# Kernel optimization log

Measured on AMD Instinct MI355X. Metric: run time of the kernel, lower is better.

The kernel has to match this reference:

```python
import jax, jax.numpy as jnp
from jax import lax
import numpy as np

D_MODEL = 128
N_HEADS = 8
N_POINTS = 8
MAX_MAG = 10.0
NEG_SLOPE = 0.1


def conv2d(x, w, b, pad):
    # x: (N, Cin, H, W), w: (Cout, Cin, kh, kw)
    y = lax.conv_general_dilated(x, w, (1, 1), [(pad, pad), (pad, pad)],
                                 dimension_numbers=('NCHW', 'OIHW', 'NCHW'))
    return y + b[None, :, None, None]


def leaky(x):
    return jnp.where(x >= 0, x, NEG_SLOPE * x)


def bilinear_sample(img, grid):
    # img: (B, C, H, W); grid: (B, P, H, W, 2) in [-1, 1] (x, y)
    # Matches torch F.grid_sample(mode='bilinear', padding_mode='zeros', align_corners=False)
    B, C, H, W = img.shape
    x = ((grid[..., 0] + 1.0) * W - 1.0) * 0.5
    y = ((grid[..., 1] + 1.0) * H - 1.0) * 0.5
    x0 = jnp.floor(x)
    y0 = jnp.floor(y)
    wx1 = x - x0
    wy1 = y - y0

    def one(img_b, x0b, y0b, wx1b, wy1b):
        def gather(xi, yi):
            valid = (xi >= 0) & (xi < W) & (yi >= 0) & (yi < H)
            xc = jnp.clip(xi, 0, W - 1).astype(jnp.int32)
            yc = jnp.clip(yi, 0, H - 1).astype(jnp.int32)
            v = img_b[:, yc, xc]  # (C, P, H, W)
            return v * valid
        wx0b = 1.0 - wx1b
        wy0b = 1.0 - wy1b
        v00 = gather(x0b, y0b)
        v01 = gather(x0b + 1, y0b)
        v10 = gather(x0b, y0b + 1)
        v11 = gather(x0b + 1, y0b + 1)
        return (v00 * (wx0b * wy0b) + v01 * (wx1b * wy0b)
                + v10 * (wx0b * wy1b) + v11 * (wx1b * wy1b))

    return jax.vmap(one)(img, x0, y0, wx1, wy1)  # (B, C, P, H, W)


def ss_deform_attn(value, loc):
    # value: (N, nh, d, H, W); loc: (N, nh, P, H, W, 2) in normalized [0,1] coords
    N, nh, d, H, W = value.shape
    P = loc.shape[2]
    v = value.reshape(N * nh, d, H, W)
    grids = (2.0 * loc - 1.0).reshape(N * nh, P, H, W, 2)
    sampled = bilinear_sample(v, grids)  # (N*nh, d, P, H, W)
    # per-location attention logits = <sampled_point, value_at_location>
    scores = jnp.einsum('ndphw,ndhw->nphw', sampled, v)
    aw = jax.nn.softmax(scores, axis=1)
    out = jnp.einsum('ndphw,nphw->ndhw', sampled, aw)
    return out.reshape(N, nh * d, H, W)


def _forward(query, value, reference_points, co_w1, co_b1, co_w2, co_b2,
             co_w3, co_b3, co_w4, co_b4, val_w, val_b, out_w, out_b):
    N, C, H, W = value.shape
    v = conv2d(value, val_w, val_b, 0)
    v = v.reshape(N, N_HEADS, D_MODEL // N_HEADS, H, W)
    o = leaky(conv2d(query, co_w1, co_b1, 1))
    o = leaky(conv2d(o, co_w2, co_b2, 1))
    o = leaky(conv2d(o, co_w3, co_b3, 1))
    o = conv2d(o, co_w4, co_b4, 1)
    o = MAX_MAG * jnp.tanh(o)
    offsets = o.reshape(N, N_HEADS, N_POINTS, H, W, 2)
    norm = jnp.array([W, H], dtype=o.dtype)  # (x, y) normalizer
    loc = reference_points[:, None, None, :, :, :] + offsets / norm
    out = ss_deform_attn(v, loc)
    return conv2d(out, out_w, out_b, 0)


def setup_inputs() -> dict:
    key = jax.random.key(0)
    ks = jax.random.split(key, 12)
    N, H, W = 4, 80, 80

    def w_init(k, shape):
        fan_in = shape[1] * shape[2] * shape[3]
        return jax.random.normal(k, shape, jnp.float32) / np.sqrt(fan_in)

    return {
        'query': jax.random.normal(ks[0], (N, 2 * D_MODEL, H, W), jnp.float32),
        'value': jax.random.normal(ks[1], (N, D_MODEL, H, W), jnp.float32),
        'reference_points': jax.random.uniform(ks[2], (N, H, W, 2), jnp.float32),
        'co_w1': w_init(ks[3], (D_MODEL, 2 * D_MODEL, 3, 3)),
        'co_b1': jnp.zeros((D_MODEL,), jnp.float32),
        'co_w2': w_init(ks[4], (D_MODEL, D_MODEL, 3, 3)),
        'co_b2': jnp.zeros((D_MODEL,), jnp.float32),
        'co_w3': w_init(ks[5], (D_MODEL, D_MODEL, 3, 3)),
        'co_b3': jnp.zeros((D_MODEL,), jnp.float32),
        'co_w4': w_init(ks[6], (N_HEADS * N_POINTS * 2, D_MODEL, 3, 3)),
        'co_b4': jnp.zeros((N_HEADS * N_POINTS * 2,), jnp.float32),
        'val_w': w_init(ks[7], (D_MODEL, D_MODEL, 1, 1)),
        'val_b': jnp.zeros((D_MODEL,), jnp.float32),
        'out_w': w_init(ks[8], (D_MODEL, D_MODEL, 1, 1)),
        'out_b': jnp.zeros((D_MODEL,), jnp.float32),
    }


def reference(query, value, reference_points, co_w1, co_b1, co_w2, co_b2,
              co_w3, co_b3, co_w4, co_b4, val_w, val_b, out_w, out_b):
    return _forward(query, value, reference_points, co_w1, co_b1, co_w2, co_b2,
                    co_w3, co_b3, co_w4, co_b4, val_w, val_b, out_w, out_b)
```

## Files before the change

### kernel.cpp

```cpp
#include <hip/hip_runtime.h>
#include <math.h>

#define Hh 80
#define Ww 80
#define HW 6400
#define PS 6724
#define NB 4

typedef _Float16 half8 __attribute__((ext_vector_type(8)));
typedef _Float16 half4v __attribute__((ext_vector_type(4)));
typedef float f32x16 __attribute__((ext_vector_type(16)));

__device__ __forceinline__ void gload16(const _Float16* g, _Float16* l) {
    __builtin_amdgcn_global_load_lds(
        (const __attribute__((address_space(1))) void*)g,
        (__attribute__((address_space(3))) void*)l, 16, 0, 0);
}

#define WAITVM(N) asm volatile("s_waitcnt vmcnt(" #N ")" ::: "memory")

__device__ __forceinline__ void barrier_mem() {
    asm volatile("" ::: "memory");
    __builtin_amdgcn_s_barrier();
    asm volatile("" ::: "memory");
}

__device__ inline void wblob_one(const float* src, _Float16* dst, int CI, int d) {
    int NC = CI / 32;
    int j = d & 7;
    int l = (d >> 3) & 63;
    int h = (d >> 9) & 1;
    int rest = d >> 10;
    int tap = rest % 9;
    rest /= 9;
    int c = rest % NC;
    int CT = rest / NC;
    int co = CT * 32 + (l & 31);
    int ci = c * 32 + h * 16 + (l >> 5) * 8 + j;
    dst[d] = (_Float16)src[((size_t)co * CI + ci) * 9 + tap];
}

__device__ inline void wblob1x1_one(const float* src, _Float16* dst, int d) {
    int j = d & 7;
    int l = (d >> 3) & 63;
    int c = (d >> 9) & 7;
    int CT = d >> 12;
    int co = CT * 32 + (l & 31);
    int ci = c * 16 + (l >> 5) * 8 + j;
    dst[d] = (_Float16)src[co * 128 + ci];
}

__device__ inline int padsite(int p) {
    if (p < 82) return p;
    if (p < 164) return 81 * 82 + (p - 82);
    if (p < 244) return (p - 163) * 82;
    return (p - 243) * 82 + 81;
}

__global__ void prep_kernel(const float* __restrict__ w1, const float* __restrict__ w2,
                            const float* __restrict__ w3, const float* __restrict__ w4,
                            const float* __restrict__ vw, const float* __restrict__ ow,
                            _Float16* __restrict__ b1, _Float16* __restrict__ b2,
                            _Float16* __restrict__ b3, _Float16* __restrict__ b4,
                            _Float16* __restrict__ bv, _Float16* __restrict__ bo,
                            int* __restrict__ qh_i, int* __restrict__ hA_i,
                            int* __restrict__ hB_i) {
    int idx = blockIdx.x * 256 + threadIdx.x;
    if (idx < 294912) { wblob_one(w1, b1, 256, idx); return; }
    idx -= 294912;
    if (idx < 147456) { wblob_one(w2, b2, 128, idx); return; }
    idx -= 147456;
    if (idx < 147456) { wblob_one(w3, b3, 128, idx); return; }
    idx -= 147456;
    if (idx < 147456) { wblob_one(w4, b4, 128, idx); return; }
    idx -= 147456;
    if (idx < 16384) { wblob1x1_one(vw, bv, idx); return; }
    idx -= 16384;
    if (idx < 16384) { wblob1x1_one(ow, bo, idx); return; }
    idx -= 16384;
    if (idx < 165888) {
        int n = idx / 41472, rr = idx % 41472;
        int c = rr / 5184, r2 = rr % 5184;
        int p = r2 >> 4, k = r2 & 15;
        qh_i[((size_t)(n * 8 + c) * PS + padsite(p)) * 16 + k] = 0;
        return;
    }
    idx -= 165888;
    if (idx < 82944) {
        int n = idx / 20736, rr = idx % 20736;
        int c = rr / 5184, r2 = rr % 5184;
        int p = r2 >> 4, k = r2 & 15;
        hA_i[((size_t)(n * 4 + c) * PS + padsite(p)) * 16 + k] = 0;
        return;
    }
    idx -= 82944;
    if (idx < 82944) {
        int n = idx / 20736, rr = idx % 20736;
        int c = rr / 5184, r2 = rr % 5184;
        int p = r2 >> 4, k = r2 & 15;
        hB_i[((size_t)(n * 4 + c) * PS + padsite(p)) * 16 + k] = 0;
    }
}

__global__ __launch_bounds__(256) void q_transpose(
    const float* __restrict__ in, _Float16* __restrict__ out) {
    const int b = blockIdx.x;
    const int xcd = b & 7, n = xcd & 3, hi = xcd >> 2;
    const int s0 = hi * 3200 + (b >> 3) * 64;
    const int t = threadIdx.x;
    constexpr int CI = 256, ST = CI + 8;
    __shared__ _Float16 T[64 * ST];
    for (int idx = t; idx < 64 * CI; idx += 256) {
        int ci = idx >> 6, sl = idx & 63;
        T[sl * ST + ci] = (_Float16)in[((size_t)n * CI + ci) * HW + s0 + sl];
    }
    __syncthreads();
    for (int idx = t; idx < 64 * 32; idx += 256) {
        int q = idx & 31, sl = idx >> 5;
        int s = s0 + sl, yy = s / 80, xx = s % 80;
        int c = q >> 2, off = (q & 3) * 8;
        *(int4*)(out + ((size_t)(n * 8 + c) * PS + (yy + 1) * 82 + (xx + 1)) * 32 + off) =
            *(const int4*)(&T[sl * ST + q * 8]);
    }
}

__global__ __launch_bounds__(256) void v_transpose(
    const float* __restrict__ in, _Float16* __restrict__ out) {
    const int b = blockIdx.x;
    const int xcd = b & 7, n = xcd & 3, hi = xcd >> 2;
    const int s0 = hi * 3200 + (b >> 3) * 64;
    const int t = threadIdx.x;
    constexpr int CI = 128, ST = CI + 8;
    __shared__ _Float16 T[64 * ST];
    for (int idx = t; idx < 64 * CI; idx += 256) {
        int ci = idx >> 6, sl = idx & 63;
        T[sl * ST + ci] = (_Float16)in[((size_t)n * CI + ci) * HW + s0 + sl];
    }
    __syncthreads();
    for (int idx = t; idx < 64 * 16; idx += 256) {
        int q = idx & 15, sl = idx >> 4;
        *(int4*)(out + ((size_t)n * HW + s0 + sl) * CI + q * 8) =
            *(const int4*)(&T[sl * ST + q * 8]);
    }
}

template <int NCp, int ACT>
__global__ __launch_bounds__(256, 2) void conv3x3_mfma(
    const _Float16* __restrict__ in, const _Float16* __restrict__ wblob,
    const float* __restrict__ bias, void* __restrict__ outp) {
    constexpr int NS = NCp * 18;
    __shared__ _Float16 Abuf[2][24 * 512];
    __shared__ _Float16 Bbuf[2][6 * 1024];

    const int b = blockIdx.x;
    const int xcd = b & 7, n = xcd & 3, hi = xcd >> 2;
    const int r = b >> 3;
    const int x0 = (r % 5) * 16, y0 = hi * 40 + (r / 5) * 4;
    const int t = threadIdx.x;
    const int w = t >> 6, l = t & 63;
    const int lane31 = l & 31, lhalf = l >> 5;
    const int lx = lane31 & 15, lyw = lane31 >> 4;
    const int si = l & 15, g8 = l >> 4;

    const _Float16* bplane0 = in + (size_t)(n * NCp) * PS * 32;
    const _Float16* wA = wblob + (size_t)w * NS * 512 + l * 8;

    f32x16 acc0 = {}, acc1 = {};

    auto stageA = [&](int grp) {
        const _Float16* asrc = wA + (size_t)grp * 6 * 512;
        _Float16* adst = &Abuf[grp & 1][w * 512];
#pragma unroll
        for (int k2 = 0; k2 < 6; ++k2)
            gload16(asrc + (size_t)k2 * 512, adst + (size_t)(k2 * 4) * 512);
    };
    auto stageB = [&](const _Float16* plane, int par) {
#pragma unroll
        for (int j = 0; j < 3; ++j) {
            const int m = 3 * w + j, rr = m >> 1, sg = m & 1;
            gload16(plane + ((size_t)((y0 + rr) * 82 + x0 + sg * 16 + si)) * 32 + g8 * 8,
                    &Bbuf[par][rr * 1024 + sg * 512]);
        }
    };
    auto compute6 = [&](int gi, const _Float16* ab, const _Float16* bb) {
#pragma unroll
        for (int k = 0; k < 6; ++k) {
            const int u = gi * 6 + k;
            const int tap = u >> 1, h = u & 1;
            const int dy = tap / 3, dx = tap % 3;
            half8 a = *(const half8*)&ab[(k * 4 + w) * 512 + l * 8];
            const int cx = lx + dx;
            const int boff = (cx >> 4) * 512 + (h * 2 + lhalf) * 128 + (cx & 15) * 8;
            half8 b0 = *(const half8*)&bb[(lyw + dy) * 1024 + boff];
            half8 b1 = *(const half8*)&bb[(lyw + 2 + dy) * 1024 + boff];
            acc0 = __builtin_amdgcn_mfma_f32_32x32x16_f16(a, b0, acc0, 0, 0, 0);
            acc1 = __builtin_amdgcn_mfma_f32_32x32x16_f16(a, b1, acc1, 0, 0, 0);
        }
    };

    stageA(0);
    stageB(bplane0, 0);

    const _Float16* bplane = bplane0;
#pragma unroll 1
    for (int c = 0; c < NCp - 1; ++c) {
        const _Float16* bplaneN = bplane + (size_t)PS * 32;
        const _Float16* bb = Bbuf[c & 1];
        stageA(3 * c + 1);
        WAITVM(6);
        barrier_mem();
        compute6(0, Abuf[(3 * c) & 1], bb);
        barrier_mem();
        stageA(3 * c + 2);
        WAITVM(6);
        barrier_mem();
        compute6(1, Abuf[(3 * c + 1) & 1], bb);
        barrier_mem();
        stageA(3 * c + 3);
        stageB(bplaneN, (c + 1) & 1);
        WAITVM(9);
        barrier_mem();
        compute6(2, Abuf[(3 * c + 2) & 1], bb);
        barrier_mem();
        bplane = bplaneN;
    }
    {
        const int c = NCp - 1;
        const _Float16* bb = Bbuf[c & 1];
        stageA(3 * c + 1);
        WAITVM(6);
        barrier_mem();
        compute6(0, Abuf[(3 * c) & 1], bb);
        barrier_mem();
        stageA(3 * c + 2);
        WAITVM(6);
        barrier_mem();
        compute6(1, Abuf[(3 * c + 1) & 1], bb);
        barrier_mem();
        WAITVM(0);
        barrier_mem();
        compute6(2, Abuf[(3 * c + 2) & 1], bb);
    }

    const int x = x0 + lx;
#pragma unroll
    for (int f = 0; f < 2; ++f) {
        const f32x16& acc = f ? acc1 : acc0;
        const int y = y0 + lyw + 2 * f;
#pragma unroll
        for (int q = 0; q < 4; ++q) {
            const int inner = 8 * q + 4 * lhalf;
            const int co0 = w * 32 + inner;
            float v[4];
#pragma unroll
            for (int i = 0; i < 4; ++i) {
                float vv = acc[q * 4 + i] + bias[co0 + i];
                if (ACT == 1) vv = (vv >= 0.f) ? vv : 0.1f * vv;
                else vv = 10.f * tanhf(vv);
                v[i] = vv;
            }
            if (ACT == 1) {
                half4v hv = {(_Float16)v[0], (_Float16)v[1], (_Float16)v[2], (_Float16)v[3]};
                *(half4v*)((_Float16*)outp +
                    ((size_t)(n * 4 + w) * PS + (y + 1) * 82 + (x + 1)) * 32 + inner) = hv;
            } else {
                float4 fv = {v[0], v[1], v[2], v[3]};
                *(float4*)((float*)outp + ((size_t)n * HW + y * 80 + x) * 128 + co0) = fv;
            }
        }
    }
}

template <int MODE>
__global__ __launch_bounds__(256) void conv1x1_mfma(
    const _Float16* __restrict__ in, const _Float16* __restrict__ wblob,
    const float* __restrict__ bias, float* __restrict__ outp) {
    const int b = blockIdx.x;
    const int xcd = b & 7, n = xcd & 3, hi = xcd >> 2;
    const int r = b >> 3;
    const int coH = r & 1, strip = r >> 1;
    const int t = threadIdx.x;
    const int w = t >> 6, l = t & 63;
    const int lane31 = l & 31, lhalf = l >> 5;
    const int s = hi * 3200 + strip * 128 + w * 32 + lane31;

    const _Float16* pB = in + (size_t)(n * HW + s) * 128 + lhalf * 8;
    const _Float16* pA0 = wblob + (size_t)(coH * 2) * 8 * 512 + l * 8;
    const _Float16* pA1 = pA0 + 8 * 512;

    half8 bB[8], bA0[8], bA1[8];
#pragma unroll
    for (int c = 0; c < 8; ++c) {
        bB[c]  = *(const half8*)(pB + c * 16);
        bA0[c] = *(const half8*)(pA0 + (size_t)c * 512);
        bA1[c] = *(const half8*)(pA1 + (size_t)c * 512);
    }
    f32x16 acc0 = {}, acc1 = {};
#pragma unroll
    for (int c = 0; c < 8; ++c) {
        acc0 = __builtin_amdgcn_mfma_f32_32x32x16_f16(bA0[c], bB[c], acc0, 0, 0, 0);
        acc1 = __builtin_amdgcn_mfma_f32_32x32x16_f16(bA1[c], bB[c], acc1, 0, 0, 0);
    }

#pragma unroll
    for (int ct = 0; ct < 2; ++ct) {
        const f32x16& acc = ct ? acc1 : acc0;
#pragma unroll
        for (int q = 0; q < 4; ++q) {
            const int co0 = coH * 64 + ct * 32 + 8 * q + 4 * lhalf;
            if (MODE == 0) {
                const int hd = co0 >> 4, dd = co0 & 15;
                float4 fv = {acc[4 * q + 0] + bias[co0 + 0], acc[4 * q + 1] + bias[co0 + 1],
                             acc[4 * q + 2] + bias[co0 + 2], acc[4 * q + 3] + bias[co0 + 3]};
                *(float4*)&outp[((size_t)(n * 8 + hd) * HW + s) * 16 + dd] = fv;
            } else {
#pragma unroll
                for (int i = 0; i < 4; ++i)
                    outp[(size_t)(n * 128 + co0 + i) * HW + s] = acc[4 * q + i] + bias[co0 + i];
            }
        }
    }
}

__global__ __launch_bounds__(256, 2) void deform_attn_kernel(
    const float* __restrict__ v_s, const float* __restrict__ offs,
    const float* __restrict__ ref, _Float16* __restrict__ att) {
    const int slice = blockIdx.x;
    const int n = slice >> 3, hd = slice & 7;
    const int t = threadIdx.x;
    const int s = blockIdx.y * 64 + (t >> 2);
    const int d0 = (t & 3) * 4;
    const int nb = n * 8 + hd;
    const float* vbase = v_s + (size_t)nb * (HW * 16) + d0;

    const float4 cv = *(const float4*)&v_s[((size_t)nb * HW + s) * 16 + d0];
    const float rx = ref[(size_t)(n * HW + s) * 2 + 0] * 80.f - 0.5f;
    const float ry = ref[(size_t)(n * HW + s) * 2 + 1] * 80.f - 0.5f;

    const int e = (s >= 3200) ? 1 : 0;
    const float* ob0 = offs + ((size_t)n * HW + (2 * s - e * HW)) * 128 + hd * 16 + e;

    float4 oxv[4], oyv[4];
#pragma unroll
    for (int i = 0; i < 4; ++i) {
        oxv[i] = *(const float4*)(ob0 + i * 4);
        oyv[i] = *(const float4*)(ob0 + 128 + i * 4);
    }
    float ox[8], oy[8];
#pragma unroll
    for (int i = 0; i < 4; ++i) {
        ox[2 * i] = oxv[i].x; ox[2 * i + 1] = oxv[i].z;
        oy[2 * i] = oyv[i].x; oy[2 * i + 1] = oyv[i].z;
    }

    float wx1[8], wy1[8];
    int ix[8], iy[8];
#pragma unroll
    for (int p = 0; p < 8; ++p) {
        const float px = rx + ox[p];
        const float py = ry + oy[p];
        const float fx = floorf(px), fy = floorf(py);
        ix[p] = (int)fx; iy[p] = (int)fy;
        wx1[p] = px - fx; wy1[p] = py - fy;
    }

    float4 g[8][4];
#pragma unroll
    for (int p = 0; p < 8; ++p) {
        const int xc0 = min(max(ix[p], 0), 79),     xc1 = min(max(ix[p] + 1, 0), 79);
        const int yc0 = min(max(iy[p], 0), 79),     yc1 = min(max(iy[p] + 1, 0), 79);
        const int r0 = yc0 * 80, r1 = yc1 * 80;
        g[p][0] = *(const float4*)(vbase + (size_t)(r0 + xc0) * 16);
        g[p][1] = *(const float4*)(vbase + (size_t)(r0 + xc1) * 16);
        g[p][2] = *(const float4*)(vbase + (size_t)(r1 + xc0) * 16);
        g[p][3] = *(const float4*)(vbase + (size_t)(r1 + xc1) * 16);
    }

    float4 sampled[8];
    float score[8];
#pragma unroll
    for (int p = 0; p < 8; ++p) {
        const float vx0 = (ix[p] >= 0 && ix[p] < Ww) ? 1.f : 0.f;
        const float vx1 = (ix[p] + 1 >= 0 && ix[p] + 1 < Ww) ? 1.f : 0.f;
        const float vy0 = (iy[p] >= 0 && iy[p] < Hh) ? 1.f : 0.f;
        const float vy1 = (iy[p] + 1 >= 0 && iy[p] + 1 < Hh) ? 1.f : 0.f;
        const float wx0 = 1.f - wx1[p], wy0 = 1.f - wy1[p];
        const float w00 = wx0 * wy0 * vx0 * vy0;
        const float w01 = wx1[p] * wy0 * vx1 * vy0;
        const float w10 = wx0 * wy1[p] * vx0 * vy1;
        const float w11 = wx1[p] * wy1[p] * vx1 * vy1;
        float4 sv;
        sv.x = g[p][0].x * w00 + g[p][1].x * w01 + g[p][2].x * w10 + g[p][3].x * w11;
        sv.y = g[p][0].y * w00 + g[p][1].y * w01 + g[p][2].y * w10 + g[p][3].y * w11;
        sv.z = g[p][0].z * w00 + g[p][1].z * w01 + g[p][2].z * w10 + g[p][3].z * w11;
        sv.w = g[p][0].w * w00 + g[p][1].w * w01 + g[p][2].w * w10 + g[p][3].w * w11;
        sampled[p] = sv;
        float sc = sv.x * cv.x + sv.y * cv.y + sv.z * cv.z + sv.w * cv.w;
        sc += __shfl_xor(sc, 1);
        sc += __shfl_xor(sc, 2);
        score[p] = sc;
    }

    float m = score[0];
#pragma unroll
    for (int p = 1; p < 8; ++p) m = fmaxf(m, score[p]);
    float sum = 0.f, aw[8];
#pragma unroll
    for (int p = 0; p < 8; ++p) {
        aw[p] = __expf(score[p] - m);
        sum += aw[p];
    }
    const float inv = 1.f / sum;
    float4 o = {0.f, 0.f, 0.f, 0.f};
#pragma unroll
    for (int p = 0; p < 8; ++p) {
        o.x += aw[p] * sampled[p].x;
        o.y += aw[p] * sampled[p].y;
        o.z += aw[p] * sampled[p].z;
        o.w += aw[p] * sampled[p].w;
    }
    o.x *= inv; o.y *= inv; o.z *= inv; o.w *= inv;

    half4v hv = {(_Float16)o.x, (_Float16)o.y, (_Float16)o.z, (_Float16)o.w};
    *(half4v*)&att[((size_t)n * HW + s) * 128 + hd * 16 + d0] = hv;
}

extern "C" void kernel_launch(void* const* d_in, const int* in_sizes, int n_in,
                              void* d_out, int out_size, void* d_ws, size_t ws_size,
                              hipStream_t stream) {
    const float* query = (const float*)d_in[0];
    const float* value = (const float*)d_in[1];
    const float* ref   = (const float*)d_in[2];
    const float* co_w1 = (const float*)d_in[3];
    const float* co_b1 = (const float*)d_in[4];
    const float* co_w2 = (const float*)d_in[5];
    const float* co_b2 = (const float*)d_in[6];
    const float* co_w3 = (const float*)d_in[7];
    const float* co_b3 = (const float*)d_in[8];
    const float* co_w4 = (const float*)d_in[9];
    const float* co_b4 = (const float*)d_in[10];
    const float* val_w = (const float*)d_in[11];
    const float* val_b = (const float*)d_in[12];
    const float* out_w = (const float*)d_in[13];
    const float* out_b = (const float*)d_in[14];

    char* ws = (char*)d_ws;
    size_t o = 0;
    auto alloc = [&](size_t bytes) { char* p = ws + o; o += (bytes + 255) & ~(size_t)255; return p; };

    _Float16* wb2 = (_Float16*)alloc(147456 * 2);
    _Float16* wb3 = (_Float16*)alloc(147456 * 2);
    _Float16* wb4 = (_Float16*)alloc(147456 * 2);
    _Float16* wbv = (_Float16*)alloc(16384 * 2);
    _Float16* wbo = (_Float16*)alloc(16384 * 2);
    char* vsR = alloc(3276800 * 4);
    float* v_s = (float*)vsR;
    _Float16* wb1 = (_Float16*)vsR;
    _Float16* v_h = (_Float16*)alloc((size_t)NB * HW * 128 * 2);
    char* R1 = alloc((size_t)NB * 8 * PS * 32 * 2);
    _Float16* q_h = (_Float16*)R1;
    float* o4 = (float*)R1;
    char* R2 = alloc((size_t)NB * 4 * PS * 32 * 2 * 2);
    _Float16* hA = (_Float16*)R2;
    _Float16* hB = (_Float16*)(R2 + (size_t)NB * 4 * PS * 32 * 2);
    _Float16* att_h = (_Float16*)R2;

    prep_kernel<<<4304, 256, 0, stream>>>(co_w1, co_w2, co_w3, co_w4, val_w, out_w,
                                          wb1, wb2, wb3, wb4, wbv, wbo,
                                          (int*)q_h, (int*)hA, (int*)hB);

    q_transpose<<<400, 256, 0, stream>>>(query, q_h);
    v_transpose<<<400, 256, 0, stream>>>(value, v_h);

    conv3x3_mfma<8, 1><<<400, 256, 0, stream>>>(q_h, wb1, co_b1, hA);

    conv1x1_mfma<0><<<400, 256, 0, stream>>>(v_h, wbv, val_b, v_s);

    conv3x3_mfma<4, 1><<<400, 256, 0, stream>>>(hA, wb2, co_b2, hB);
    conv3x3_mfma<4, 1><<<400, 256, 0, stream>>>(hB, wb3, co_b3, hA);
    conv3x3_mfma<4, 2><<<400, 256, 0, stream>>>(hA, wb4, co_b4, o4);

    deform_attn_kernel<<<dim3(32, 100), 256, 0, stream>>>(v_s, o4, ref, att_h);

    conv1x1_mfma<1><<<400, 256, 0, stream>>>(att_h, wbo, out_b, (float*)d_out);
}
```

Measured before the change: 234.2 us.

## Load conv weights directly into registers and pair-unroll the chunk loop

```diff
diff --git a/kernel.cpp b/kernel.cpp
--- a/kernel.cpp
+++ b/kernel.cpp
@@ -149,7 +149,7 @@
     const _Float16* __restrict__ in, const _Float16* __restrict__ wblob,
     const float* __restrict__ bias, void* __restrict__ outp) {
     constexpr int NS = NCp * 18;
-    __shared__ _Float16 Abuf[2][24 * 512];
+    static_assert((NCp & 1) == 0, "pair-unrolled chunk loop needs even NCp");
     __shared__ _Float16 Bbuf[2][6 * 1024];
 
     const int b = blockIdx.x;
@@ -167,13 +167,6 @@
 
     f32x16 acc0 = {}, acc1 = {};
 
-    auto stageA = [&](int grp) {
-        const _Float16* asrc = wA + (size_t)grp * 6 * 512;
-        _Float16* adst = &Abuf[grp & 1][w * 512];
-#pragma unroll
-        for (int k2 = 0; k2 < 6; ++k2)
-            gload16(asrc + (size_t)k2 * 512, adst + (size_t)(k2 * 4) * 512);
-    };
     auto stageB = [&](const _Float16* plane, int par) {
 #pragma unroll
         for (int j = 0; j < 3; ++j) {
@@ -182,64 +175,53 @@
                     &Bbuf[par][rr * 1024 + sg * 512]);
         }
     };
-    auto compute6 = [&](int gi, const _Float16* ab, const _Float16* bb) {
-#pragma unroll
-        for (int k = 0; k < 6; ++k) {
-            const int u = gi * 6 + k;
+    auto loadA = [&](int c, half8 (&ar)[18]) {
+        const _Float16* asrc = wA + (size_t)c * 18 * 512;
+#pragma unroll
+        for (int u = 0; u < 18; ++u)
+            ar[u] = *(const half8*)(asrc + (size_t)u * 512);
+    };
+    auto compute18 = [&](const _Float16* bb, const half8 (&ar)[18]) {
+#pragma unroll
+        for (int u = 0; u < 18; ++u) {
             const int tap = u >> 1, h = u & 1;
             const int dy = tap / 3, dx = tap % 3;
-            half8 a = *(const half8*)&ab[(k * 4 + w) * 512 + l * 8];
             const int cx = lx + dx;
             const int boff = (cx >> 4) * 512 + (h * 2 + lhalf) * 128 + (cx & 15) * 8;
             half8 b0 = *(const half8*)&bb[(lyw + dy) * 1024 + boff];
             half8 b1 = *(const half8*)&bb[(lyw + 2 + dy) * 1024 + boff];
-            acc0 = __builtin_amdgcn_mfma_f32_32x32x16_f16(a, b0, acc0, 0, 0, 0);
-            acc1 = __builtin_amdgcn_mfma_f32_32x32x16_f16(a, b1, acc1, 0, 0, 0);
+            acc0 = __builtin_amdgcn_mfma_f32_32x32x16_f16(ar[u], b0, acc0, 0, 0, 0);
+            acc1 = __builtin_amdgcn_mfma_f32_32x32x16_f16(ar[u], b1, acc1, 0, 0, 0);
         }
     };
 
-    stageA(0);
+    half8 aX[18], aY[18];
+
     stageB(bplane0, 0);
+    loadA(0, aX);
+    WAITVM(0);
+    barrier_mem();
 
     const _Float16* bplane = bplane0;
 #pragma unroll 1
-    for (int c = 0; c < NCp - 1; ++c) {
-        const _Float16* bplaneN = bplane + (size_t)PS * 32;
-        const _Float16* bb = Bbuf[c & 1];
-        stageA(3 * c + 1);
-        WAITVM(6);
-        barrier_mem();
-        compute6(0, Abuf[(3 * c) & 1], bb);
-        barrier_mem();
-        stageA(3 * c + 2);
-        WAITVM(6);
-        barrier_mem();
-        compute6(1, Abuf[(3 * c + 1) & 1], bb);
-        barrier_mem();
-        stageA(3 * c + 3);
-        stageB(bplaneN, (c + 1) & 1);
-        WAITVM(9);
-        barrier_mem();
-        compute6(2, Abuf[(3 * c + 2) & 1], bb);
-        barrier_mem();
-        bplane = bplaneN;
-    }
-    {
-        const int c = NCp - 1;
-        const _Float16* bb = Bbuf[c & 1];
-        stageA(3 * c + 1);
-        WAITVM(6);
-        barrier_mem();
-        compute6(0, Abuf[(3 * c) & 1], bb);
-        barrier_mem();
-        stageA(3 * c + 2);
-        WAITVM(6);
-        barrier_mem();
-        compute6(1, Abuf[(3 * c + 1) & 1], bb);
-        barrier_mem();
+    for (int cp = 0; cp < NCp / 2; ++cp) {
+        const int c0 = 2 * cp;
+        stageB(bplane + (size_t)PS * 32, 1);
+        loadA(c0 + 1, aY);
+        compute18(Bbuf[0], aX);
         WAITVM(0);
         barrier_mem();
-        compute6(2, Abuf[(3 * c + 2) & 1], bb);
+        bplane += (size_t)PS * 32;
+        if (c0 + 2 < NCp) {
+            stageB(bplane + (size_t)PS * 32, 0);
+            loadA(c0 + 2, aX);
+            compute18(Bbuf[1], aY);
+            WAITVM(0);
+            barrier_mem();
+        } else {
+            compute18(Bbuf[1], aY);
+        }
+        bplane += (size_t)PS * 32;
     }
 
     const int x = x0 + lx;
```

After: 293.0 us. +25.1%, slower.
